# Optimization experiments

Hardware: AMD Instinct MI355X
Metric: run time of the kernel (lower is better)

The kernel has to match this reference:

```python
import jax, jax.numpy as jnp
import numpy as np

CH = 256
NH = 8
HD = CH // NH  # 32


def setup_inputs() -> dict:
    key = jax.random.key(0)
    k1, k2, k3, k4 = jax.random.split(key, 4)
    x = jax.random.normal(k1, (2, CH, 16, 16, 16), dtype=jnp.float32)
    # 1x1x1 Conv3d weights == per-voxel linear maps over channels
    qkv_w = jax.random.normal(k2, (3 * CH, CH), dtype=jnp.float32) * (1.0 / np.sqrt(CH))
    proj_w = jax.random.normal(k3, (CH, CH), dtype=jnp.float32) * (1.0 / np.sqrt(CH))
    proj_b = jax.random.normal(k4, (CH,), dtype=jnp.float32) * 0.01
    return {"x": x, "qkv_w": qkv_w, "proj_w": proj_w, "proj_b": proj_b}


def reference(x, qkv_w, proj_w, proj_b):
    B, C, D, H, W = x.shape
    N = D * H * W
    nh, hd = NH, HD
    xf = x.reshape(B, C, N)  # [B, C, N]
    # qkv 1x1x1 conv: [B, 3C, N]
    qkv = jnp.einsum('oc,bcn->bon', qkv_w, xf)
    # split channel dim as (3, nh, hd), then arrange to [3, B, nh, N, hd]
    qkv = qkv.reshape(B, 3, nh, hd, N).transpose(1, 0, 2, 4, 3)
    q, k, v = qkv[0], qkv[1], qkv[2]
    scale = hd ** -0.5
    attn = jnp.einsum('bhqd,bhkd->bhqk', q, k) * scale  # [B, nh, N, N]
    attn = jax.nn.softmax(attn, axis=-1)
    # dropout is identity in eval mode
    out = jnp.einsum('bhqk,bhkd->bhqd', attn, v)  # [B, nh, N, hd]
    out = out.transpose(0, 1, 3, 2).reshape(B, C, D, H, W)
    out = jnp.einsum('oc,bcdhw->bodhw', proj_w, out) + proj_b[None, :, None, None, None]
    return out
```

## Files before the change

### kernel.cpp

```cpp
#include <hip/hip_runtime.h>
#include <hip/hip_bf16.h>

typedef __bf16 bf16;
typedef __bf16 bf16x8 __attribute__((ext_vector_type(8)));
typedef float f32x4 __attribute__((ext_vector_type(4)));
typedef float f32x16 __attribute__((ext_vector_type(16)));
typedef unsigned int u32x4 __attribute__((ext_vector_type(4)));

#define EXP2(x) __builtin_amdgcn_exp2f(x)

static __device__ __forceinline__ f32x4 mfma16(bf16x8 a, bf16x8 b, f32x4 c) {
    return __builtin_amdgcn_mfma_f32_16x16x32_bf16(a, b, c, 0, 0, 0);
}
static __device__ __forceinline__ f32x16 mfma32(bf16x8 a, bf16x8 b, f32x16 c) {
    return __builtin_amdgcn_mfma_f32_32x32x16_bf16(a, b, c, 0, 0, 0);
}
static __device__ __forceinline__ unsigned cvt_pk(float lo, float hi) {
    unsigned r;
    asm("v_cvt_pk_bf16_f32 %0, %1, %2" : "=v"(r) : "v"(lo), "v"(hi));
    return r;
}
static __device__ __forceinline__ void perm32swap(unsigned &a, unsigned &b) {
    asm("v_permlane32_swap_b32 %0, %1" : "+v"(a), "+v"(b));
}

__global__ __launch_bounds__(256) void prep_w_kernel(const float* __restrict__ qkv_w,
                                                     const float* __restrict__ proj_w,
                                                     bf16* __restrict__ wqkv,
                                                     bf16* __restrict__ wproj) {
    int idx = blockIdx.x * 256 + threadIdx.x;
    const float QSCALE = 0.17677669529663689f * 1.4426950408889634f;
    if (idx < 768 * 256) {
        float v = qkv_w[idx];
        if (idx < 256 * 256) v *= QSCALE;
        wqkv[idx] = (bf16)v;
    } else {
        int j = idx - 768 * 256;
        wproj[j] = (bf16)proj_w[j];
    }
}

__global__ __launch_bounds__(256) void transpose_x_kernel(const float* __restrict__ x,
                                                          bf16* __restrict__ xT) {
    __shared__ float tile[32][33];
    int b = blockIdx.z, cb = blockIdx.y * 32, nb = blockIdx.x * 32;
    int t = threadIdx.x;
    int tn = t & 31, tc = t >> 5;
    const float* src = x + ((size_t)b * 256 + cb) * 4096 + nb;
#pragma unroll
    for (int i = 0; i < 4; i++)
        tile[tc + i * 8][tn] = src[(size_t)(tc + i * 8) * 4096 + tn];
    __syncthreads();
    bf16* dst = xT + ((size_t)b * 4096 + nb) * 256 + cb;
#pragma unroll
    for (int i = 0; i < 4; i++)
        dst[(size_t)(tc + i * 8) * 256 + tn] = (bf16)tile[tn][tc + i * 8];
}

__global__ __launch_bounds__(256) void qkv_gemm_kernel(const bf16* __restrict__ xT,
                                                       const bf16* __restrict__ w,
                                                       bf16* __restrict__ Q,
                                                       bf16* __restrict__ Kp,
                                                       bf16* __restrict__ Vp) {
    int b = blockIdx.z;
    int nb = blockIdx.x * 128, ob = blockIdx.y * 128;
    int t = threadIdx.x, wid = t >> 6, lane = t & 63;
    int l15 = lane & 15, g = lane >> 4;
    int wr = wid >> 1, wc = wid & 1;
    const bf16* xrow = xT + ((size_t)b * 4096 + nb + wr * 64 + l15) * 256 + g * 8;
    const bf16* wrow = w + (size_t)(ob + wc * 64 + l15) * 256 + g * 8;
    f32x4 acc[4][4] = {};
    for (int k0 = 0; k0 < 256; k0 += 32) {
        bf16x8 a[4], bb[4];
#pragma unroll
        for (int rt = 0; rt < 4; rt++) a[rt] = *(const bf16x8*)(xrow + rt * 16 * 256 + k0);
#pragma unroll
        for (int cg = 0; cg < 4; cg++) bb[cg] = *(const bf16x8*)(wrow + cg * 16 * 256 + k0);
#pragma unroll
        for (int rt = 0; rt < 4; rt++)
#pragma unroll
            for (int cg = 0; cg < 4; cg++)
                acc[rt][cg] = mfma16(a[rt], bb[cg], acc[rt][cg]);
    }
#pragma unroll
    for (int rt = 0; rt < 4; rt++) {
#pragma unroll
        for (int cg = 0; cg < 4; cg++) {
            int o = ob + wc * 64 + cg * 16 + l15;
            int tsel = o >> 8;
            int h = (o >> 5) & 7;
            int d = o & 31;
            int n0 = nb + wr * 64 + rt * 16 + g * 4;
            size_t bhbase = ((size_t)b * 8 + h) * 131072;
            if (tsel == 0) {
#pragma unroll
                for (int i = 0; i < 4; i++)
                    Q[(((size_t)b * 8 + h) * 4096 + n0 + i) * 32 + d] = (bf16)acc[rt][cg][i];
            } else if (tsel == 1) {
                int kt = n0 >> 5;
                int which = d >> 4, hi2 = (d >> 3) & 1, j = d & 7;
                size_t base = bhbase + (size_t)(((kt * 2 + which) * 64 + hi2 * 32) * 8 + j);
#pragma unroll
                for (int i = 0; i < 4; i++) {
                    int r5 = (n0 + i) & 31;
                    Kp[base + r5 * 8] = (bf16)acc[rt][cg][i];
                }
            } else {
                int kt = n0 >> 5, kk0 = n0 & 31;
                int which = kk0 >> 4, hi2 = (kk0 >> 3) & 1, j0 = kk0 & 7;
                unsigned p0 = cvt_pk(acc[rt][cg][0], acc[rt][cg][1]);
                unsigned p1 = cvt_pk(acc[rt][cg][2], acc[rt][cg][3]);
                uint2 wv; wv.x = p0; wv.y = p1;
                *(uint2*)(Vp + bhbase + (size_t)(((kt * 2 + which) * 64 + hi2 * 32 + d) * 8 + j0)) = wv;
            }
        }
    }
}

#define PACK(stv, B, OUT) {                                  \
    unsigned _x01 = cvt_pk(stv[B + 0], stv[B + 1]);          \
    unsigned _x23 = cvt_pk(stv[B + 2], stv[B + 3]);          \
    unsigned _y01 = cvt_pk(stv[B + 4], stv[B + 5]);          \
    unsigned _y23 = cvt_pk(stv[B + 6], stv[B + 7]);          \
    perm32swap(_x01, _y01);                                  \
    perm32swap(_x23, _y23);                                  \
    u32x4 _w = {_x01, _x23, _y01, _y23};                     \
    OUT = __builtin_bit_cast(bf16x8, _w); }

__global__ __launch_bounds__(512, 4) void attn_kernel(const bf16* __restrict__ Q,
                                                      const bf16* __restrict__ Kp,
                                                      const bf16* __restrict__ Vp,
                                                      bf16* __restrict__ attT) {
    __shared__ __align__(16) float ldsO[4][64][20];
    __shared__ float ldsL[4][32];

    const int bh = blockIdx.y;
    const int t = threadIdx.x;
    const int wid = t >> 6, lane = t & 63;
    const int z = wid >> 2, wq = wid & 3;
    const int l31 = lane & 31, hi = lane >> 5;
    const int q0 = blockIdx.x * 128 + wq * 32;

    const bf16* __restrict__ Qb = Q + (size_t)bh * 4096 * 32;
    const bf16* kptr = Kp + (size_t)bh * 131072 + (size_t)z * 65536 + lane * 8;
    const bf16* vptr = Vp + (size_t)bh * 131072 + (size_t)z * 65536 + lane * 8;

    bf16x8 qf0 = *(const bf16x8*)(Qb + (size_t)(q0 + l31) * 32 + hi * 8);
    bf16x8 qf1 = *(const bf16x8*)(Qb + (size_t)(q0 + l31) * 32 + 16 + hi * 8);

    bf16x8 ones;
#pragma unroll
    for (int j = 0; j < 8; j++) ones[j] = (bf16)1.0f;

    f32x16 o_acc = {};
    f32x16 rs = {};

    bf16x8 kf0 = *(const bf16x8*)(kptr);
    bf16x8 kf1 = *(const bf16x8*)(kptr + 512);

    for (int it = 0; it < 64; ++it) {
        bf16x8 vf0 = *(const bf16x8*)(vptr);
        bf16x8 vf1 = *(const bf16x8*)(vptr + 512);
        vptr += 1024;

        f32x16 zz = {};
        f32x16 st = mfma32(kf0, qf0, zz);
        st = mfma32(kf1, qf1, st);

        kptr += 1024;
        bf16x8 kf0n = *(const bf16x8*)(kptr);
        bf16x8 kf1n = *(const bf16x8*)(kptr + 512);

#pragma unroll
        for (int r = 0; r < 16; r++) st[r] = EXP2(st[r]);

        bf16x8 pb0, pb1;
        PACK(st, 0, pb0);
        PACK(st, 8, pb1);

        rs = mfma32(ones, pb0, rs);
        o_acc = mfma32(vf0, pb0, o_acc);
        rs = mfma32(ones, pb1, rs);
        o_acc = mfma32(vf1, pb1, o_acc);

        kf0 = kf0n; kf1 = kf1n;
    }

    if (z == 1) {
#pragma unroll
        for (int g = 0; g < 4; g++) {
            f32x4 wv = {o_acc[4 * g + 0], o_acc[4 * g + 1], o_acc[4 * g + 2], o_acc[4 * g + 3]};
            *(f32x4*)&ldsO[wq][lane][4 * g] = wv;
        }
        if (hi == 0) ldsL[wq][l31] = rs[0];
    }
    __syncthreads();
    if (z == 0) {
        float inv = __builtin_amdgcn_rcpf(rs[0] + ldsL[wq][l31]);
        const int b = bh >> 3, h = bh & 7;
        bf16* orow = attT + ((size_t)b * 4096 + q0 + l31) * 256 + h * 32 + 4 * hi;
#pragma unroll
        for (int g = 0; g < 4; g++) {
            f32x4 p = *(const f32x4*)&ldsO[wq][lane][4 * g];
            unsigned w0 = cvt_pk((o_acc[4 * g + 0] + p[0]) * inv, (o_acc[4 * g + 1] + p[1]) * inv);
            unsigned w1 = cvt_pk((o_acc[4 * g + 2] + p[2]) * inv, (o_acc[4 * g + 3] + p[3]) * inv);
            uint2 w;
            w.x = w0; w.y = w1;
            *(uint2*)(orow + 8 * g) = w;
        }
    }
}

__global__ __launch_bounds__(256) void proj_gemm_kernel(const bf16* __restrict__ attT,
                                                        const bf16* __restrict__ w,
                                                        const float* __restrict__ bias,
                                                        float* __restrict__ out) {
    int b = blockIdx.z;
    int nb = blockIdx.x * 128, ob = blockIdx.y * 64;
    int t = threadIdx.x, wid = t >> 6, lane = t & 63;
    int l15 = lane & 15, g = lane >> 4;
    int wr = wid >> 1, wc = wid & 1;
    const bf16* arow = w + (size_t)(ob + wr * 32 + l15) * 256 + g * 8;
    const bf16* brow = attT + ((size_t)b * 4096 + nb + wc * 64 + l15) * 256 + g * 8;
    f32x4 acc[2][4] = {};
    for (int k0 = 0; k0 < 256; k0 += 32) {
        bf16x8 a[2], bb[4];
#pragma unroll
        for (int rt = 0; rt < 2; rt++) a[rt] = *(const bf16x8*)(arow + rt * 16 * 256 + k0);
#pragma unroll
        for (int cg = 0; cg < 4; cg++) bb[cg] = *(const bf16x8*)(brow + cg * 16 * 256 + k0);
#pragma unroll
        for (int rt = 0; rt < 2; rt++)
#pragma unroll
            for (int cg = 0; cg < 4; cg++)
                acc[rt][cg] = mfma16(a[rt], bb[cg], acc[rt][cg]);
    }
#pragma unroll
    for (int rt = 0; rt < 2; rt++)
#pragma unroll
        for (int cg = 0; cg < 4; cg++)
#pragma unroll
            for (int i = 0; i < 4; i++) {
                int o = ob + wr * 32 + rt * 16 + g * 4 + i;
                int n = nb + wc * 64 + cg * 16 + l15;
                out[((size_t)b * 256 + o) * 4096 + n] = acc[rt][cg][i] + bias[o];
            }
}

extern "C" void kernel_launch(void* const* d_in, const int* in_sizes, int n_in,
                              void* d_out, int out_size, void* d_ws, size_t ws_size,
                              hipStream_t stream) {
    const float* x      = (const float*)d_in[0];
    const float* qkv_w  = (const float*)d_in[1];
    const float* proj_w = (const float*)d_in[2];
    const float* proj_b = (const float*)d_in[3];
    float* out = (float*)d_out;

    char* ws = (char*)d_ws;
    bf16* xT    = (bf16*)(ws);
    bf16* wqkv  = (bf16*)(ws + 4194304);
    bf16* wproj = (bf16*)(ws + 4587520);
    bf16* Qb    = (bf16*)(ws + 4718592);
    bf16* Kp    = (bf16*)(ws + 8912896);
    bf16* Vp    = (bf16*)(ws + 13107200);
    bf16* attT  = (bf16*)(ws + 17301504);

    prep_w_kernel<<<1024, 256, 0, stream>>>(qkv_w, proj_w, wqkv, wproj);
    transpose_x_kernel<<<dim3(128, 8, 2), 256, 0, stream>>>(x, xT);
    qkv_gemm_kernel<<<dim3(32, 6, 2), 256, 0, stream>>>(xT, wqkv, Qb, Kp, Vp);
    attn_kernel<<<dim3(32, 16), 512, 0, stream>>>(Qb, Kp, Vp, attT);
    proj_gemm_kernel<<<dim3(32, 4, 2), 256, 0, stream>>>(attT, wproj, proj_b, out);
}
```

Measured before the change: 95.94 us.

## Unroll attention loop by two with deeper K/V prefetch, setprio, and block remap

The attention main loop is unrolled by two, and both K and V for the next step are loaded a full iteration ahead, so global loads have more time to arrive before use. The MFMA accumulation section is wrapped in s_setprio to favour matrix issue across waves. The grid is flattened and remapped so that consecutive blocks walk across heads before query blocks, which changes L2 locality for K/V. Launch bounds are loosened from 4 to 2 blocks per CU, allowing more registers for the extra prefetch at some cost in occupancy.

```diff
diff --git a/kernel.cpp b/kernel.cpp
--- a/kernel.cpp
+++ b/kernel.cpp
@@ -127,19 +127,36 @@
     u32x4 _w = {_x01, _x23, _y01, _y23};                     \
     OUT = __builtin_bit_cast(bf16x8, _w); }
 
-__global__ __launch_bounds__(512, 4) void attn_kernel(const bf16* __restrict__ Q,
+#define BODY(KF0, KF1, VF0, VF1) {                           \
+    f32x16 st = mfma32(KF0, qf0, ZERO16);                    \
+    st = mfma32(KF1, qf1, st);                               \
+    _Pragma("unroll")                                        \
+    for (int r = 0; r < 16; r++) st[r] = EXP2(st[r]);        \
+    bf16x8 pb0, pb1;                                         \
+    PACK(st, 0, pb0);                                        \
+    PACK(st, 8, pb1);                                        \
+    __builtin_amdgcn_s_setprio(1);                           \
+    rs = mfma32(ones, pb0, rs);                              \
+    o_acc = mfma32(VF0, pb0, o_acc);                         \
+    rs = mfma32(ones, pb1, rs);                              \
+    o_acc = mfma32(VF1, pb1, o_acc);                         \
+    __builtin_amdgcn_s_setprio(0); }
+
+__global__ __launch_bounds__(512, 2) void attn_kernel(const bf16* __restrict__ Q,
                                                       const bf16* __restrict__ Kp,
                                                       const bf16* __restrict__ Vp,
                                                       bf16* __restrict__ attT) {
     __shared__ __align__(16) float ldsO[4][64][20];
     __shared__ float ldsL[4][32];
 
-    const int bh = blockIdx.y;
+    const int w = blockIdx.x;
+    const int bh = (w & 7) + 8 * ((w >> 3) & 1);
+    const int qblk = w >> 4;
     const int t = threadIdx.x;
     const int wid = t >> 6, lane = t & 63;
     const int z = wid >> 2, wq = wid & 3;
     const int l31 = lane & 31, hi = lane >> 5;
-    const int q0 = blockIdx.x * 128 + wq * 32;
+    const int q0 = qblk * 128 + wq * 32;
 
     const bf16* __restrict__ Qb = Q + (size_t)bh * 4096 * 32;
     const bf16* kptr = Kp + (size_t)bh * 131072 + (size_t)z * 65536 + lane * 8;
@@ -151,39 +168,28 @@
     bf16x8 ones;
 #pragma unroll
     for (int j = 0; j < 8; j++) ones[j] = (bf16)1.0f;
+    const f32x16 ZERO16 = {};
 
     f32x16 o_acc = {};
     f32x16 rs = {};
 
     bf16x8 kf0 = *(const bf16x8*)(kptr);
     bf16x8 kf1 = *(const bf16x8*)(kptr + 512);
-
-    for (int it = 0; it < 64; ++it) {
-        bf16x8 vf0 = *(const bf16x8*)(vptr);
-        bf16x8 vf1 = *(const bf16x8*)(vptr + 512);
-        vptr += 1024;
-
-        f32x16 zz = {};
-        f32x16 st = mfma32(kf0, qf0, zz);
-        st = mfma32(kf1, qf1, st);
-
-        kptr += 1024;
-        bf16x8 kf0n = *(const bf16x8*)(kptr);
-        bf16x8 kf1n = *(const bf16x8*)(kptr + 512);
-
-#pragma unroll
-        for (int r = 0; r < 16; r++) st[r] = EXP2(st[r]);
-
-        bf16x8 pb0, pb1;
-        PACK(st, 0, pb0);
-        PACK(st, 8, pb1);
-
-        rs = mfma32(ones, pb0, rs);
-        o_acc = mfma32(vf0, pb0, o_acc);
-        rs = mfma32(ones, pb1, rs);
-        o_acc = mfma32(vf1, pb1, o_acc);
-
-        kf0 = kf0n; kf1 = kf1n;
+    bf16x8 vf0 = *(const bf16x8*)(vptr);
+    bf16x8 vf1 = *(const bf16x8*)(vptr + 512);
+
+    for (int it = 0; it < 64; it += 2) {
+        bf16x8 kn0 = *(const bf16x8*)(kptr + 1024);
+        bf16x8 kn1 = *(const bf16x8*)(kptr + 1536);
+        bf16x8 vn0 = *(const bf16x8*)(vptr + 1024);
+        bf16x8 vn1 = *(const bf16x8*)(vptr + 1536);
+        BODY(kf0, kf1, vf0, vf1);
+        kf0 = *(const bf16x8*)(kptr + 2048);
+        kf1 = *(const bf16x8*)(kptr + 2560);
+        vf0 = *(const bf16x8*)(vptr + 2048);
+        vf1 = *(const bf16x8*)(vptr + 2560);
+        kptr += 2048; vptr += 2048;
+        BODY(kn0, kn1, vn0, vn1);
     }
 
     if (z == 1) {
@@ -204,9 +210,9 @@
             f32x4 p = *(const f32x4*)&ldsO[wq][lane][4 * g];
             unsigned w0 = cvt_pk((o_acc[4 * g + 0] + p[0]) * inv, (o_acc[4 * g + 1] + p[1]) * inv);
             unsigned w1 = cvt_pk((o_acc[4 * g + 2] + p[2]) * inv, (o_acc[4 * g + 3] + p[3]) * inv);
-            uint2 w;
-            w.x = w0; w.y = w1;
-            *(uint2*)(orow + 8 * g) = w;
+            uint2 wv;
+            wv.x = w0; wv.y = w1;
+            *(uint2*)(orow + 8 * g) = wv;
         }
     }
 }
@@ -268,6 +274,6 @@
     prep_w_kernel<<<1024, 256, 0, stream>>>(qkv_w, proj_w, wqkv, wproj);
     transpose_x_kernel<<<dim3(128, 8, 2), 256, 0, stream>>>(x, xT);
     qkv_gemm_kernel<<<dim3(32, 6, 2), 256, 0, stream>>>(xT, wqkv, Qb, Kp, Vp);
-    attn_kernel<<<dim3(32, 16), 512, 0, stream>>>(Qb, Kp, Vp, attT);
+    attn_kernel<<<512, 512, 0, stream>>>(Qb, Kp, Vp, attT);
     proj_gemm_kernel<<<dim3(32, 4, 2), 256, 0, stream>>>(attT, wproj, proj_b, out);
 }
```

Measured after the change: 95.46 us. No clear change (-0.5%).
